# Kernel tuning notes

Measured on AMD Instinct MI355X. Metric: run time of the kernel, lower is better.

## Reference

```python
import jax, jax.numpy as jnp
import numpy as np

H, W, NUM_HEADS = 32, 32, 8


def dwconv3x3(x, w, b):
    # x: (B,C,H,W), w: (C,1,3,3) depthwise, b: (C,)
    y = jax.lax.conv_general_dilated(
        x, w, window_strides=(1, 1), padding='SAME',
        dimension_numbers=('NCHW', 'OIHW', 'NCHW'),
        feature_group_count=x.shape[1])
    return y + b[None, :, None, None]


def conv1x1(x, w, b):
    # x: (B,C,H,W), w: (O,C), b: (O,)
    return jnp.einsum('oc,bchw->bohw', w, x) + b[None, :, None, None]


def layernorm(x, w, b, eps=1e-6):
    mu = x.mean(-1, keepdims=True)
    var = ((x - mu) ** 2).mean(-1, keepdims=True)
    return (x - mu) / jnp.sqrt(var + eps) * w + b


def setup_inputs() -> dict:
    key = jax.random.key(0)
    ks = jax.random.split(key, 12)
    B, N, C = 32, H * W, 512
    Ch = 4 * C  # inverted MLP hidden
    s_lin = 0.02
    s_dw = np.sqrt(2.0 / 9.0)   # fan_out init for 3x3 depthwise
    s_pw1 = np.sqrt(2.0 / Ch)
    s_pw2 = np.sqrt(2.0 / C)
    return {
        'x': jax.random.normal(ks[0], (B, N, C), jnp.float32),
        'cpe_w': jax.random.normal(ks[1], (C, 1, 3, 3), jnp.float32) * s_dw,
        'cpe_b': jnp.zeros((C,), jnp.float32),
        'ln1_w': jnp.ones((C,), jnp.float32),
        'ln1_b': jnp.zeros((C,), jnp.float32),
        'qkv_w': jax.random.normal(ks[2], (3 * C, C), jnp.float32) * s_lin,
        'crpe_w': jax.random.normal(ks[3], (C, 1, 3, 3), jnp.float32) * s_dw,
        'crpe_b': jnp.zeros((C,), jnp.float32),
        'ln2_w': jnp.ones((C,), jnp.float32),
        'ln2_b': jnp.zeros((C,), jnp.float32),
        'fc1_w': jax.random.normal(ks[4], (Ch, C), jnp.float32) * s_pw1,
        'fc1_b': jnp.zeros((Ch,), jnp.float32),
        'dw_w': jax.random.normal(ks[5], (Ch, 1, 3, 3), jnp.float32) * s_dw,
        'dw_b': jnp.zeros((Ch,), jnp.float32),
        'fc2_w': jax.random.normal(ks[6], (C, Ch), jnp.float32) * s_pw2,
        'fc2_b': jnp.zeros((C,), jnp.float32),
    }


def reference(x, cpe_w, cpe_b, ln1_w, ln1_b, qkv_w, crpe_w, crpe_b,
              ln2_w, ln2_b, fc1_w, fc1_b, dw_w, dw_b, fc2_w, fc2_b):
    B, N, C = x.shape
    h = NUM_HEADS
    d = C // h
    scale = d ** -0.5

    # --- Convolutional position encoding: x = x + dwconv(x) ---
    img = x.reshape(B, H, W, C).transpose(0, 3, 1, 2)  # B C H W
    img = img + dwconv3x3(img, cpe_w, cpe_b)
    x = img.transpose(0, 2, 3, 1).reshape(B, N, C)

    # --- Factorized attention + conv relative position encoding ---
    cur = layernorm(x, ln1_w, ln1_b)
    qkv = cur @ qkv_w.T                                 # (B,N,3C)
    qkv = qkv.reshape(B, N, 3, h, d).transpose(2, 0, 3, 1, 4)  # (3,B,h,N,d)
    q, k, v = qkv[0], qkv[1], qkv[2]
    k_softmax = jax.nn.softmax(k, axis=2)               # softmax over tokens N
    ktv = jnp.einsum('bhnk,bhnv->bhkv', k_softmax, v)   # (B,h,d,d)
    factor_att = jnp.einsum('bhnk,bhkv->bhnv', q, ktv)  # (B,h,N,d)
    # crpe: depthwise conv on v as image, elementwise-multiplied by q
    v_img = v.transpose(0, 1, 3, 2).reshape(B, h * d, H, W)
    v_img = dwconv3x3(v_img, crpe_w, crpe_b)
    v_conv = v_img.reshape(B, h, d, N).transpose(0, 1, 3, 2)
    crpe = q * v_conv
    attn_out = (scale * factor_att + crpe).transpose(0, 2, 1, 3).reshape(B, N, C)
    x = x + attn_out

    # --- Inverted MLP (conv-based channel mixing) ---
    cur = layernorm(x, ln2_w, ln2_b)
    img = cur.reshape(B, H, W, C).transpose(0, 3, 1, 2)  # B C H W
    hdn = conv1x1(img, fc1_w, fc1_b)
    hdn = jax.nn.gelu(hdn, approximate=False)
    hdn = hdn + dwconv3x3(hdn, dw_w, dw_b)
    out = conv1x1(hdn, fc2_w, fc2_b)
    x = x + out.transpose(0, 2, 3, 1).reshape(B, N, C)
    return x
```

## Files before the change

### kernel.cpp

```cpp
#include <hip/hip_runtime.h>
#include <hip/hip_bf16.h>

using bf16 = __hip_bfloat16;
using s16x4 = __attribute__((ext_vector_type(4))) short;
using s16x8 = __attribute__((ext_vector_type(8))) short;
using f32x4 = __attribute__((ext_vector_type(4))) float;

#define DI __device__ __forceinline__

template <int N> DI void wvm() {
    if constexpr (N == 8) asm volatile("s_waitcnt vmcnt(8)" ::: "memory");
    else if constexpr (N == 4) asm volatile("s_waitcnt vmcnt(4)" ::: "memory");
    else if constexpr (N == 2) asm volatile("s_waitcnt vmcnt(2)" ::: "memory");
    else if constexpr (N == 1) asm volatile("s_waitcnt vmcnt(1)" ::: "memory");
    else asm volatile("s_waitcnt vmcnt(0)" ::: "memory");
}

DI float b2f(short s) { union { unsigned u; float f; } z; z.u = ((unsigned)(unsigned short)s) << 16; return z.f; }
DI short f2b(float f) { bf16 t = __float2bfloat16(f); return *(short*)&t; }

DI float gelu_f(float x) {
    const float t = 0.7978845608f * x * (1.f + 0.044715f * x * x);
    const float e = __expf(2.f * t);
    const float th = 1.f - 2.f / (e + 1.f);
    return 0.5f * x * (1.f + th);
}

DI void ld8(const bf16* p, float* f) {
    s16x8 x = *(const s16x8*)(const void*)p;
#pragma unroll
    for (int c = 0; c < 8; c++) f[c] = b2f(x[c]);
}
DI void ld8(const float* p, float* f) {
    float4 a = *(const float4*)p, b = *(const float4*)(p + 4);
    f[0]=a.x; f[1]=a.y; f[2]=a.z; f[3]=a.w; f[4]=b.x; f[5]=b.y; f[6]=b.z; f[7]=b.w;
}

typedef const __attribute__((address_space(1))) void* gp_t;
typedef __attribute__((address_space(3))) void* lp_t;
DI void gload_lds16(const void* g, void* l) {
    __builtin_amdgcn_global_load_lds((gp_t)g, (lp_t)l, 16, 0, 0);
}

__global__ void diag_k(float* out, float v) { out[0] = v; }

__global__ void f2bf_k(const float* __restrict__ in, bf16* __restrict__ out, int n) {
    int i = (blockIdx.x * 256 + threadIdx.x) * 8;
    if (i >= n) return;
    float f[8];
    ld8(in + i, f);
    s16x8 o;
#pragma unroll
    for (int c = 0; c < 8; c++) o[c] = f2b(f[c]);
    *(s16x8*)(void*)(out + i) = o;
}

DI void tap10(const float* r, float w0, float w1, float w2, float* acc) {
#pragma unroll
    for (int i = 0; i < 8; i++)
        acc[i] += w0 * r[i] + w1 * r[i + 1] + w2 * r[i + 2];
}

template <typename TI, typename TO, bool RESID, int CPL>
__global__ __launch_bounds__(256) void conv4_k(
    const TI* in, long rs, long coff,
    const float* __restrict__ w, const float* __restrict__ bias,
    TO* out, long ors, int gshift)
{
    constexpr int CH = 64 * CPL;
    constexpr int ECNT = CH / 8;
    __shared__ float buf[2][CH][33];
    const int t = threadIdx.x;
    const int band = blockIdx.x & 3;
    const int cg = (blockIdx.x >> 2) & ((1 << gshift) - 1);
    const int img = blockIdx.x >> (2 + gshift);
    const int y0 = band * 8;

    const int spx = t >> 3;
    const int sce = (t & 7) * ECNT;
    const TI* gsrc = in + ((long)img << 10) * rs + coff + (long)cg * CH + sce;

    const int c = t & 63;
    const int xb = (t >> 6) * 8;

    float wv9[9][CPL], bw[CPL];
#pragma unroll
    for (int p = 0; p < CPL; p++) {
        const int gch = cg * CH + c * CPL + p;
#pragma unroll
        for (int j = 0; j < 9; j++) wv9[j][p] = w[gch * 9 + j];
        bw[p] = bias[gch];
    }

    auto stage = [&](int row) {
        float f[ECNT];
        ld8(gsrc + (long)(row * 32 + spx) * rs, f);
        if constexpr (ECNT == 16) ld8(gsrc + (long)(row * 32 + spx) * rs + 8, f + 8);
        float* d = &buf[row & 1][0][0];
#pragma unroll
        for (int k = 0; k < ECNT; k++) {
            const int ch = sce + k;
            const int rr = (CPL == 2) ? ((ch & 1) * 64 + (ch >> 1)) : ch;
            d[rr * 33 + spx] = f[k];
        }
    };
    auto slice = [&](int row, float r[CPL][10]) {
#pragma unroll
        for (int p = 0; p < CPL; p++) {
            const float* s = &buf[row & 1][c + p * 64][0];
            r[p][0] = (xb == 0) ? 0.f : s[xb - 1];
#pragma unroll
            for (int i = 0; i < 8; i++) r[p][1 + i] = s[xb + i];
            r[p][9] = (xb + 8 >= 32) ? 0.f : s[xb + 8];
        }
    };
    auto zero = [&](float r[CPL][10]) {
#pragma unroll
        for (int p = 0; p < CPL; p++)
#pragma unroll
            for (int i = 0; i < 10; i++) r[p][i] = 0.f;
    };

    float r0[CPL][10], r1[CPL][10], r2[CPL][10];
    if (y0 > 0) stage(y0 - 1);
    __syncthreads();
    if (y0 > 0) slice(y0 - 1, r0); else zero(r0);
    stage(y0);
    __syncthreads();
    slice(y0, r1);

    for (int y = y0; y < y0 + 8; ++y) {
        const int yn = y + 1;
        if (yn <= 31) stage(yn);
        __syncthreads();
        if (yn <= 31) slice(yn, r2); else zero(r2);
        float acc[CPL][8];
#pragma unroll
        for (int p = 0; p < CPL; p++) {
#pragma unroll
            for (int i = 0; i < 8; i++) acc[p][i] = bw[p];
            tap10(r0[p], wv9[0][p], wv9[1][p], wv9[2][p], acc[p]);
            tap10(r1[p], wv9[3][p], wv9[4][p], wv9[5][p], acc[p]);
            tap10(r2[p], wv9[6][p], wv9[7][p], wv9[8][p], acc[p]);
            if (RESID) {
#pragma unroll
                for (int i = 0; i < 8; i++) acc[p][i] += r1[p][i + 1];
            }
        }
        TO* o = out + ((long)(img * 1024 + y * 32 + xb)) * ors + (long)cg * CH + c * CPL;
#pragma unroll
        for (int i = 0; i < 8; i++) {
            if constexpr (CPL == 2 && sizeof(TO) == 2) {
                const unsigned u = (unsigned)(unsigned short)f2b(acc[0][i]) |
                                   ((unsigned)(unsigned short)f2b(acc[1][i]) << 16);
                *(unsigned*)(void*)(o + (long)i * ors) = u;
            } else {
                o[(long)i * ors] = (TO)acc[0][i];
            }
        }
#pragma unroll
        for (int p = 0; p < CPL; p++)
#pragma unroll
            for (int i = 0; i < 10; i++) { r0[p][i] = r1[p][i]; r1[p][i] = r2[p][i]; }
    }
}

__global__ __launch_bounds__(256) void ln_k(const float* __restrict__ x,
                                            const float* __restrict__ w,
                                            const float* __restrict__ bp,
                                            bf16* __restrict__ out)
{
    const size_t row = blockIdx.x * 4 + (threadIdx.x >> 6);
    const int t = threadIdx.x & 63;
    const float* xr = x + row * 512;
    alignas(16) float v[8];
    *(float4*)&v[0] = *(const float4*)(xr + t * 8);
    *(float4*)&v[4] = *(const float4*)(xr + t * 8 + 4);
    float s = 0.f;
#pragma unroll
    for (int j = 0; j < 8; j++) s += v[j];
#pragma unroll
    for (int mm = 32; mm; mm >>= 1) s += __shfl_xor(s, mm);
    const float mu = s * (1.f / 512.f);
    float q = 0.f;
#pragma unroll
    for (int j = 0; j < 8; j++) { v[j] -= mu; q += v[j] * v[j]; }
#pragma unroll
    for (int mm = 32; mm; mm >>= 1) q += __shfl_xor(q, mm);
    const float rstd = rsqrtf(q * (1.f / 512.f) + 1e-6f);
    alignas(16) float wv[8], bv[8];
    *(float4*)&wv[0] = *(const float4*)(w + t * 8);
    *(float4*)&wv[4] = *(const float4*)(w + t * 8 + 4);
    *(float4*)&bv[0] = *(const float4*)(bp + t * 8);
    *(float4*)&bv[4] = *(const float4*)(bp + t * 8 + 4);
    alignas(16) bf16 o[8];
#pragma unroll
    for (int j = 0; j < 8; j++) o[j] = __float2bfloat16(v[j] * rstd * wv[j] + bv[j]);
    *(uint4*)(out + row * 512 + t * 8) = *(const uint4*)o;
}

template <int EPI, int K, int NY>
__global__ __launch_bounds__(512) void gemm8p_k(
    const bf16* __restrict__ A, const bf16* __restrict__ Bw,
    const float* __restrict__ bias, bf16* __restrict__ outb, int M, int Nn)
{
    constexpr int KT = K / 64;
    __shared__ __align__(16) char lds[131072];
    char* ldsA = lds;
    char* ldsB = lds + 65536;
    const int t = threadIdx.x;
    const int lane = t & 63;
    const int w = t >> 6;
    const int wr = w >> 2, wc = w & 3;
    const int nwg = 128 * NY;
    const int swz = (blockIdx.x & 7) * (nwg >> 3) + (blockIdx.x >> 3);
    const int m0 = (swz / NY) * 256;
    const int n0 = (swz % NY) * 256;
    const int lr = lane & 15, lg = lane >> 4;

    f32x4 acc[8][4] = {};

    const int srow = lane >> 3;
    const int ssrc = 8 * ((lane & 7) ^ srow);

    auto SA = [&](int b, int kt, int h) {
#pragma unroll
        for (int j = 0; j < 2; j++) {
            const int lrow0 = j * 64 + w * 8;
            const int R0 = j * 128 + h * 64 + (lrow0 & 63);
            gload_lds16(A + (size_t)(m0 + R0 + srow) * K + kt * 64 + ssrc,
                        ldsA + ((b * 2 + h) * 128 + lrow0) * 128);
        }
    };
    auto SB = [&](int b, int kt, int h) {
#pragma unroll
        for (int j = 0; j < 2; j++) {
            const int lrow0 = j * 64 + w * 8;
            const int R0 = (lrow0 >> 5) * 64 + h * 32 + (lrow0 & 31);
            gload_lds16(Bw + (size_t)(n0 + R0 + srow) * K + kt * 64 + ssrc,
                        ldsB + ((b * 2 + h) * 128 + lrow0) * 128);
        }
    };
    auto RA = [&](int b, int h, int m, int ks) -> s16x8 {
        return *(const s16x8*)(ldsA + ((b * 2 + h) * 128 + wr * 64 + m * 16 + lr) * 128
                               + (((ks * 4 + lg) ^ (lr & 7)) << 4));
    };
    auto RB = [&](int b, int h, int n, int ks) -> s16x8 {
        return *(const s16x8*)(ldsB + ((b * 2 + h) * 128 + wc * 32 + n * 16 + lr) * 128
                               + (((ks * 4 + lg) ^ (lr & 7)) << 4));
    };
    auto MM = [&](int mb, int nb, s16x8 (&a)[2][4], s16x8 (&b)[2][2]) {
#pragma unroll
        for (int ks = 0; ks < 2; ks++)
#pragma unroll
            for (int m = 0; m < 4; m++)
#pragma unroll
                for (int n = 0; n < 2; n++)
                    acc[mb + m][nb + n] =
                        __builtin_amdgcn_mfma_f32_16x16x32_bf16(a[ks][m], b[ks][n], acc[mb + m][nb + n], 0, 0, 0);
    };

    SA(0, 0, 0); SB(0, 0, 0); SA(0, 0, 1); SB(0, 0, 1);
    SA(1, 1, 0); SB(1, 1, 0);
    wvm<8>();
    __builtin_amdgcn_s_barrier();

    s16x8 aLo[2][4], aHi[2][4], bLo[2][2], bHi[2][2];
    auto TILE = [&](int kt) {
        const int b = kt & 1;
#pragma unroll
        for (int ks = 0; ks < 2; ks++) {
#pragma unroll
            for (int m = 0; m < 4; m++) aLo[ks][m] = RA(b, 0, m, ks);
#pragma unroll
            for (int n = 0; n < 2; n++) bLo[ks][n] = RB(b, 0, n, ks);
        }
        if (kt + 1 < KT) SA(b ^ 1, kt + 1, 1);
        __builtin_amdgcn_s_barrier();
        __builtin_amdgcn_s_setprio(1);
        MM(0, 0, aLo, bLo);
        __builtin_amdgcn_s_setprio(0);
        if (kt + 1 < KT) wvm<8>(); else wvm<2>();
        __builtin_amdgcn_s_barrier();
#pragma unroll
        for (int ks = 0; ks < 2; ks++)
#pragma unroll
            for (int m = 0; m < 4; m++) aHi[ks][m] = RA(b, 1, m, ks);
        if (kt + 1 < KT) SB(b ^ 1, kt + 1, 1);
        __builtin_amdgcn_s_barrier();
        __builtin_amdgcn_s_setprio(1);
        MM(4, 0, aHi, bLo);
        __builtin_amdgcn_s_setprio(0);
        if (kt + 1 < KT) wvm<8>(); else wvm<0>();
        __builtin_amdgcn_s_barrier();
#pragma unroll
        for (int ks = 0; ks < 2; ks++)
#pragma unroll
            for (int n = 0; n < 2; n++) bHi[ks][n] = RB(b, 1, n, ks);
        if (kt + 2 < KT) SA(b, kt + 2, 0);
        __builtin_amdgcn_s_barrier();
        __builtin_amdgcn_s_setprio(1);
        MM(4, 2, aHi, bHi);
        __builtin_amdgcn_s_setprio(0);
        __builtin_amdgcn_s_barrier();
        if (kt + 2 < KT) SB(b, kt + 2, 0);
        __builtin_amdgcn_s_barrier();
        __builtin_amdgcn_s_setprio(1);
        MM(0, 2, aLo, bHi);
        __builtin_amdgcn_s_setprio(0);
        if (kt + 2 < KT) { wvm<8>(); __builtin_amdgcn_s_barrier(); }
        else if (kt + 1 < KT) { wvm<4>(); __builtin_amdgcn_s_barrier(); }
    };

#pragma unroll
    for (int kt = 0; kt < KT; ++kt) TILE(kt);

#pragma unroll
    for (int i = 0; i < 8; i++) {
#pragma unroll
        for (int j = 0; j < 4; j++) {
            const int col = n0 + wc * 64 + j * 16 + lr;
            float bcol = 0.f;
            if constexpr (EPI >= 1) bcol = bias[col];
#pragma unroll
            for (int r = 0; r < 4; r++) {
                const int row = m0 + wr * 128 + i * 16 + lg * 4 + r;
                float v = acc[i][j][r] + bcol;
                const size_t idx = (size_t)row * Nn + col;
                outb[idx] = __float2bfloat16(EPI == 1 ? gelu_f(v) : v);
            }
        }
    }
}

__global__ __launch_bounds__(512) void gemm8ps_k(
    const bf16* __restrict__ A, const bf16* __restrict__ A2,
    const bf16* __restrict__ Bw, const float* __restrict__ bias,
    const float* resid, float* outf, int M, int Nn)
{
    constexpr int KT = 32;
    __shared__ __align__(16) char lds[65536];
    char* ldsA = lds;
    char* ldsB = lds + 32768;
    const int t = threadIdx.x;
    const int lane = t & 63;
    const int w = t >> 6;
    const int wr = w >> 2, wc = w & 3;
    const int swz = (blockIdx.x & 7) * 128 + (blockIdx.x >> 3);
    const int m0 = (swz >> 2) * 128;
    const int n0 = (swz & 3) * 128;
    const int lr = lane & 15, lg = lane >> 4;

    f32x4 acc[4][2] = {};

    const int srow = lane >> 3;
    const int ssrc = 8 * ((lane & 7) ^ srow);
    const int lrow0 = w * 8;

    auto SA = [&](int b, int kt, int h) {
        const bf16* Ab = (kt < 16) ? A : A2;
        const int ktl = (kt < 16) ? kt : kt - 16;
        const int R0 = h * 64 + lrow0;
        gload_lds16(Ab + (size_t)(m0 + R0 + srow) * 1024 + ktl * 64 + ssrc,
                    ldsA + ((b * 2 + h) * 64 + lrow0) * 128);
    };
    auto SB = [&](int b, int kt, int h) {
        const int R0 = (lrow0 >> 4) * 32 + h * 16 + (lrow0 & 15);
        gload_lds16(Bw + (size_t)(n0 + R0 + srow) * 2048 + kt * 64 + ssrc,
                    ldsB + ((b * 2 + h) * 64 + lrow0) * 128);
    };
    auto RA = [&](int b, int h, int m, int ks) -> s16x8 {
        return *(const s16x8*)(ldsA + ((b * 2 + h) * 64 + wr * 32 + m * 16 + lr) * 128
                               + (((ks * 4 + lg) ^ (lr & 7)) << 4));
    };
    auto RB = [&](int b, int h, int ks) -> s16x8 {
        return *(const s16x8*)(ldsB + ((b * 2 + h) * 64 + wc * 16 + lr) * 128
                               + (((ks * 4 + lg) ^ (lr & 7)) << 4));
    };
    auto MM = [&](int hm, int hn, s16x8 (&a)[2][2], s16x8 (&bb)[2]) {
#pragma unroll
        for (int ks = 0; ks < 2; ks++)
#pragma unroll
            for (int m = 0; m < 2; m++)
                acc[hm * 2 + m][hn] =
                    __builtin_amdgcn_mfma_f32_16x16x32_bf16(a[ks][m], bb[ks], acc[hm * 2 + m][hn], 0, 0, 0);
    };

    SA(0, 0, 0); SB(0, 0, 0); SA(0, 0, 1); SB(0, 0, 1);
    SA(1, 1, 0); SB(1, 1, 0);
    wvm<4>();
    __builtin_amdgcn_s_barrier();

    s16x8 aLo[2][2], aHi[2][2], bLo[2], bHi[2];
#pragma unroll 2
    for (int kt = 0; kt < KT; ++kt) {
        const int b = kt & 1;
#pragma unroll
        for (int ks = 0; ks < 2; ks++) {
#pragma unroll
            for (int m = 0; m < 2; m++) aLo[ks][m] = RA(b, 0, m, ks);
            bLo[ks] = RB(b, 0, ks);
        }
        if (kt + 1 < KT) SA(b ^ 1, kt + 1, 1);
        __builtin_amdgcn_s_barrier();
        __builtin_amdgcn_s_setprio(1);
        MM(0, 0, aLo, bLo);
        __builtin_amdgcn_s_setprio(0);
        if (kt + 1 < KT) wvm<4>(); else wvm<1>();
        __builtin_amdgcn_s_barrier();
#pragma unroll
        for (int ks = 0; ks < 2; ks++)
#pragma unroll
            for (int m = 0; m < 2; m++) aHi[ks][m] = RA(b, 1, m, ks);
        if (kt + 1 < KT) SB(b ^ 1, kt + 1, 1);
        __builtin_amdgcn_s_barrier();
        __builtin_amdgcn_s_setprio(1);
        MM(1, 0, aHi, bLo);
        __builtin_amdgcn_s_setprio(0);
        if (kt + 1 < KT) wvm<4>(); else wvm<0>();
        __builtin_amdgcn_s_barrier();
#pragma unroll
        for (int ks = 0; ks < 2; ks++) bHi[ks] = RB(b, 1, ks);
        if (kt + 2 < KT) SA(b, kt + 2, 0);
        __builtin_amdgcn_s_barrier();
        __builtin_amdgcn_s_setprio(1);
        MM(1, 1, aHi, bHi);
        __builtin_amdgcn_s_setprio(0);
        __builtin_amdgcn_s_barrier();
        if (kt + 2 < KT) SB(b, kt + 2, 0);
        __builtin_amdgcn_s_barrier();
        __builtin_amdgcn_s_setprio(1);
        MM(0, 1, aLo, bHi);
        __builtin_amdgcn_s_setprio(0);
        if (kt + 2 < KT) { wvm<4>(); __builtin_amdgcn_s_barrier(); }
        else if (kt + 1 < KT) { wvm<2>(); __builtin_amdgcn_s_barrier(); }
    }

#pragma unroll
    for (int mf = 0; mf < 4; mf++) {
#pragma unroll
        for (int nf = 0; nf < 2; nf++) {
            const int col = n0 + wc * 32 + nf * 16 + lr;
            const float bcol = bias[col];
#pragma unroll
            for (int r = 0; r < 4; r++) {
                const int row = m0 + (mf >> 1) * 64 + wr * 32 + (mf & 1) * 16 + lg * 4 + r;
                const size_t idx = (size_t)row * Nn + col;
                outf[idx] = acc[mf][nf][r] + bcol + resid[idx];
            }
        }
    }
}

__global__ __launch_bounds__(256) void ktv3_k(const bf16* __restrict__ qkv,
                                              float* __restrict__ ktvp,
                                              float* __restrict__ csp)
{
    __shared__ __align__(16) char P[64 * 128];
    __shared__ __align__(16) char Vt[64 * 128];
    __shared__ float csl[64 * 5];
    const int t = threadIdx.x;
    const int bh = blockIdx.x >> 1, half = blockIdx.x & 1;
    const int b = bh >> 3, hh = bh & 7;
    const int lane = t & 63, w = t >> 6;
    const int lr = lane & 15, lg = lane >> 4;

    const int n_r = t >> 2;
    const int k0 = (t & 3) * 16;
    const bf16* kbase = qkv + (size_t)(b * 1024) * 1536 + 512 + hh * 64 + k0;
    const bf16* vbase = kbase + 512;

    const int kq = t & 63, qq = t >> 6;
    float cacc = 0.f;

    f32x4 acc[4] = {};

    for (int n0 = half * 512; n0 < half * 512 + 512; n0 += 64) {
        const uint4 ka = *(const uint4*)(kbase + (size_t)(n0 + n_r) * 1536);
        const uint4 kb2 = *(const uint4*)(kbase + (size_t)(n0 + n_r) * 1536 + 8);
        const uint4 va = *(const uint4*)(vbase + (size_t)(n0 + n_r) * 1536);
        const uint4 vb2 = *(const uint4*)(vbase + (size_t)(n0 + n_r) * 1536 + 8);
        __syncthreads();
        {
            const short* ke = (const short*)&ka;
            const short* ke2 = (const short*)&kb2;
            const short* ve = (const short*)&va;
            const short* ve2 = (const short*)&vb2;
            const int nslot = ((n_r >> 3) << 4);
            const int nbyte = (n_r & 7) * 2;
#pragma unroll
            for (int j = 0; j < 16; j++) {
                const int row = k0 + j;
                const short kv = j < 8 ? ke[j] : ke2[j - 8];
                const short vv = j < 8 ? ve[j] : ve2[j - 8];
                const int off = row * 128 + (nslot ^ ((row & 7) << 4)) + nbyte;
                *(short*)(P + off) = f2b(__expf(b2f(kv)));
                *(short*)(Vt + off) = vv;
            }
        }
        __syncthreads();
        {
            const char* pr = P + kq * 128;
            const int sw = (kq & 7) << 4;
            s16x8 x0 = *(const s16x8*)(pr + (((qq * 2) << 4) ^ sw));
            s16x8 x1 = *(const s16x8*)(pr + (((qq * 2 + 1) << 4) ^ sw));
#pragma unroll
            for (int j = 0; j < 8; j++) cacc += b2f(x0[j]) + b2f(x1[j]);
        }
#pragma unroll
        for (int ks2 = 0; ks2 < 2; ks2++) {
            s16x8 aF = *(const s16x8*)(Vt + (w * 16 + lr) * 128 + (((ks2 * 4 + lg) ^ (lr & 7)) << 4));
            s16x8 bF[4];
#pragma unroll
            for (int j = 0; j < 4; j++)
                bF[j] = *(const s16x8*)(P + (j * 16 + lr) * 128 + (((ks2 * 4 + lg) ^ (lr & 7)) << 4));
#pragma unroll
            for (int j = 0; j < 4; j++)
                acc[j] = __builtin_amdgcn_mfma_f32_16x16x32_bf16(aF, bF[j], acc[j], 0, 0, 0);
        }
    }
    __syncthreads();
    csl[kq * 5 + qq] = cacc;
    __syncthreads();
    if (t < 64) csp[blockIdx.x * 64 + t] = csl[t * 5] + csl[t * 5 + 1] + csl[t * 5 + 2] + csl[t * 5 + 3];

    float* o = ktvp + (size_t)blockIdx.x * 4096;
#pragma unroll
    for (int j = 0; j < 4; j++) {
        const int col = j * 16 + lr;
#pragma unroll
        for (int r = 0; r < 4; r++) {
            const int vrow = w * 16 + lg * 4 + r;
            o[vrow * 64 + col] = acc[j][r];
        }
    }
}

__global__ __launch_bounds__(256) void ktvred2_k(const float* __restrict__ ktvp,
                                                 const float* __restrict__ csp,
                                                 bf16* __restrict__ ktvT)
{
    const int bh = blockIdx.x;
    const int t = threadIdx.x;
#pragma unroll
    for (int i = 0; i < 16; i++) {
        const int e = t + 256 * i;
        const int col = e & 63;
        const float cs = csp[(bh * 2) * 64 + col] + csp[(bh * 2 + 1) * 64 + col];
        const float val = ktvp[(size_t)(bh * 2) * 4096 + e] + ktvp[(size_t)(bh * 2 + 1) * 4096 + e];
        ktvT[(size_t)bh * 4096 + e] = __float2bfloat16(val * (0.125f / cs));
    }
}

__global__ __launch_bounds__(256) void attnout2_k(
    float* xs, const bf16* __restrict__ qkv,
    const bf16* __restrict__ ktvT, const bf16* __restrict__ vc)
{
    __shared__ __align__(16) char qs[256 * 128];
    __shared__ __align__(16) char ks[64 * 128];
    const int t = threadIdx.x;
    const int bid = blockIdx.x;
    const int b = bid >> 5, hh = (bid >> 2) & 7, nc = bid & 3;
    const int n0 = nc * 256;
    const int lane = t & 63, w = t >> 6;
    const int lr = lane & 15, lg = lane >> 4;

    {
        const int r0 = t >> 3, sl = t & 7;
#pragma unroll
        for (int it = 0; it < 8; it++) {
            const int row = it * 32 + r0;
            const uint4 v = *(const uint4*)(qkv + ((size_t)(b * 1024 + n0 + row)) * 1536 + hh * 64 + sl * 8);
            *(uint4*)(qs + row * 128 + ((sl ^ (row & 7)) << 4)) = v;
        }
#pragma unroll
        for (int it = 0; it < 2; it++) {
            const int u = it * 256 + t;
            const int vr = u >> 3, sl2 = u & 7;
            const uint4 vv = *(const uint4*)(ktvT + (size_t)(b * 8 + hh) * 4096 + vr * 64 + sl2 * 8);
            *(uint4*)(ks + vr * 128 + ((sl2 ^ (vr & 7)) << 4)) = vv;
        }
    }
    __syncthreads();

    f32x4 acc[4][4] = {};
    s16x8 aF[2][4], bF[2][4];
#pragma unroll
    for (int ksi = 0; ksi < 2; ksi++) {
#pragma unroll
        for (int m = 0; m < 4; m++) {
            const int row = w * 64 + m * 16 + lr;
            aF[ksi][m] = *(const s16x8*)(qs + row * 128 + (((ksi * 4 + lg) ^ (lr & 7)) << 4));
        }
#pragma unroll
        for (int j = 0; j < 4; j++) {
            const int vr = j * 16 + lr;
            bF[ksi][j] = *(const s16x8*)(ks + vr * 128 + (((ksi * 4 + lg) ^ (lr & 7)) << 4));
        }
    }
#pragma unroll
    for (int ksi = 0; ksi < 2; ksi++)
#pragma unroll
        for (int m = 0; m < 4; m++)
#pragma unroll
            for (int j = 0; j < 4; j++)
                acc[m][j] = __builtin_amdgcn_mfma_f32_16x16x32_bf16(aF[ksi][m], bF[ksi][j], acc[m][j], 0, 0, 0);

#pragma unroll
    for (int m = 0; m < 4; m++) {
#pragma unroll
        for (int j = 0; j < 4; j++) {
#pragma unroll
            for (int r = 0; r < 4; r++) {
                const int lrow = w * 64 + m * 16 + lg * 4 + r;
                const int col = j * 16 + lr;
                const size_t idx = ((size_t)(b * 1024 + n0 + lrow)) * 512 + hh * 64 + col;
                const short qv = *(const short*)(qs + lrow * 128 + ((((col >> 3) ^ (lrow & 7)) << 4)) + (col & 7) * 2);
                xs[idx] = xs[idx] + acc[m][j][r] + b2f(qv) * __bfloat162float(vc[idx]);
            }
        }
    }
}

static constexpr size_t OFF_WQ   = 0;
static constexpr size_t OFF_W1   = 1572864;
static constexpr size_t OFF_W2   = 3670016;
static constexpr size_t OFF_CUR  = 5767168;
static constexpr size_t OFF_H2B  = 5767168;
static constexpr size_t OFF_QKV  = 72876032;
static constexpr size_t OFF_HG   = 72876032;
static constexpr size_t OFF_VC   = 173539328;
static constexpr size_t OFF_KTVP = 173539328;
static constexpr size_t OFF_CSP  = 181927936;
static constexpr size_t OFF_H2A  = 139984896;
static constexpr size_t OFF_KTV  = 207093760;
static constexpr size_t WS_NEED  = 207618048;

extern "C" void kernel_launch(void* const* d_in, const int* in_sizes, int n_in,
                              void* d_out, int out_size, void* d_ws, size_t ws_size,
                              hipStream_t stream)
{
    const float* x     = (const float*)d_in[0];
    const float* cpe_w = (const float*)d_in[1];
    const float* cpe_b = (const float*)d_in[2];
    const float* ln1_w = (const float*)d_in[3];
    const float* ln1_b = (const float*)d_in[4];
    const float* qkv_w = (const float*)d_in[5];
    const float* crpe_w= (const float*)d_in[6];
    const float* crpe_b= (const float*)d_in[7];
    const float* ln2_w = (const float*)d_in[8];
    const float* ln2_b = (const float*)d_in[9];
    const float* fc1_w = (const float*)d_in[10];
    const float* fc1_b = (const float*)d_in[11];
    const float* dw_w  = (const float*)d_in[12];
    const float* dw_b  = (const float*)d_in[13];
    const float* fc2_w = (const float*)d_in[14];
    const float* fc2_b = (const float*)d_in[15];
    float* spine = (float*)d_out;
    char* ws = (char*)d_ws;

    if (ws_size < WS_NEED) {
        diag_k<<<1, 1, 0, stream>>>(spine, (float)ws_size);
        return;
    }

    bf16*  wq   = (bf16*)(ws + OFF_WQ);
    bf16*  w1   = (bf16*)(ws + OFF_W1);
    bf16*  w2b  = (bf16*)(ws + OFF_W2);
    bf16*  cur  = (bf16*)(ws + OFF_CUR);
    bf16*  qkv  = (bf16*)(ws + OFF_QKV);
    bf16*  vc   = (bf16*)(ws + OFF_VC);
    float* ktvp = (float*)(ws + OFF_KTVP);
    float* csp  = (float*)(ws + OFF_CSP);
    bf16*  ktvT = (bf16*)(ws + OFF_KTV);
    bf16*  hg   = (bf16*)(ws + OFF_HG);
    bf16*  h2a  = (bf16*)(ws + OFF_H2A);
    bf16*  h2b  = (bf16*)(ws + OFF_H2B);

    f2bf_k<<<(1536 * 512 / 8 + 255) / 256, 256, 0, stream>>>(qkv_w, wq, 1536 * 512);
    f2bf_k<<<(2048 * 512 / 8 + 255) / 256, 256, 0, stream>>>(fc1_w, w1, 2048 * 512);
    f2bf_k<<<(2048 * 512 / 8 + 255) / 256, 256, 0, stream>>>(fc2_w, w2b, 512 * 2048);

    conv4_k<float, float, true, 1><<<32 * 8 * 4, 256, 0, stream>>>(x, 512, 0, cpe_w, cpe_b, spine, 512, 3);

    const int M = 32768;
    ln_k<<<M / 4, 256, 0, stream>>>(spine, ln1_w, ln1_b, cur);
    gemm8p_k<0, 512, 6><<<768, 512, 0, stream>>>(cur, wq, nullptr, qkv, M, 1536);
    ktv3_k<<<512, 256, 0, stream>>>(qkv, ktvp, csp);
    ktvred2_k<<<256, 256, 0, stream>>>(ktvp, csp, ktvT);
    conv4_k<bf16, bf16, false, 2><<<32 * 4 * 4, 256, 0, stream>>>(qkv, 1536, 1024, crpe_w, crpe_b, vc, 512, 2);
    attnout2_k<<<32 * 8 * 4, 256, 0, stream>>>(spine, qkv, ktvT, vc);
    ln_k<<<M / 4, 256, 0, stream>>>(spine, ln2_w, ln2_b, cur);

    gemm8p_k<1, 512, 4><<<512, 512, 0, stream>>>(cur, w1, fc1_b, hg, M, 1024);
    conv4_k<bf16, bf16, true, 2><<<32 * 8 * 4, 256, 0, stream>>>(hg, 1024, 0, dw_w, dw_b, h2a, 1024, 3);
    gemm8p_k<1, 512, 4><<<512, 512, 0, stream>>>(cur, w1 + (size_t)1024 * 512, fc1_b + 1024, hg, M, 1024);
    conv4_k<bf16, bf16, true, 2><<<32 * 8 * 4, 256, 0, stream>>>(hg, 1024, 0, dw_w + (size_t)1024 * 9, dw_b + 1024, h2b, 1024, 3);
    gemm8ps_k<<<1024, 512, 0, stream>>>(h2a, h2b, w2b, fc2_b, spine, spine, M, 512);
}
```

Before: 466.6 us.

## Generalize split-K GEMM for fc1 tiles and fold KtV reduction into attention output

Templates the 128x128 gemm8ps kernel over epilogue, K, tile grid and dual-A input, and uses it for both fc1 GEMMs with 2048 workgroups in place of the larger-tile kernel. Removes the separate ktvred kernel: attnout now sums the two partial KtV halves and normalizes by the column sums while loading into LDS. This drops a launch and a bf16 intermediate, but repeats the reduction work in every block that touches the same head. Workspace offsets for the partials now alias the cur buffer, which relies on kernel ordering.

Measured after the change: 465.6 us. About the same (-0.2%).

```diff
diff --git a/kernel.cpp b/kernel.cpp
--- a/kernel.cpp
+++ b/kernel.cpp
@@ -333,12 +333,14 @@
     }
 }
 
+template <int EPI, int K, int NY, bool DUAL>
 __global__ __launch_bounds__(512) void gemm8ps_k(
     const bf16* __restrict__ A, const bf16* __restrict__ A2,
     const bf16* __restrict__ Bw, const float* __restrict__ bias,
-    const float* resid, float* outf, int M, int Nn)
+    const float* resid, bf16* __restrict__ outb, float* outf, int M, int Nn)
 {
-    constexpr int KT = 32;
+    constexpr int KT = K / 64;
+    constexpr int LDA = DUAL ? K / 2 : K;
     __shared__ __align__(16) char lds[65536];
     char* ldsA = lds;
     char* ldsB = lds + 32768;
@@ -346,9 +348,10 @@
     const int lane = t & 63;
     const int w = t >> 6;
     const int wr = w >> 2, wc = w & 3;
-    const int swz = (blockIdx.x & 7) * 128 + (blockIdx.x >> 3);
-    const int m0 = (swz >> 2) * 128;
-    const int n0 = (swz & 3) * 128;
+    const int nwg = gridDim.x;
+    const int swz = (blockIdx.x & 7) * (nwg >> 3) + (blockIdx.x >> 3);
+    const int m0 = (swz / NY) * 128;
+    const int n0 = (swz % NY) * 128;
     const int lr = lane & 15, lg = lane >> 4;
 
     f32x4 acc[4][2] = {};
@@ -358,15 +361,16 @@
     const int lrow0 = w * 8;
 
     auto SA = [&](int b, int kt, int h) {
-        const bf16* Ab = (kt < 16) ? A : A2;
-        const int ktl = (kt < 16) ? kt : kt - 16;
+        const bf16* Ab = A;
+        int ktl = kt;
+        if constexpr (DUAL) { if (kt >= KT / 2) { Ab = A2; ktl = kt - KT / 2; } }
         const int R0 = h * 64 + lrow0;
-        gload_lds16(Ab + (size_t)(m0 + R0 + srow) * 1024 + ktl * 64 + ssrc,
+        gload_lds16(Ab + (size_t)(m0 + R0 + srow) * LDA + ktl * 64 + ssrc,
                     ldsA + ((b * 2 + h) * 64 + lrow0) * 128);
     };
     auto SB = [&](int b, int kt, int h) {
         const int R0 = (lrow0 >> 4) * 32 + h * 16 + (lrow0 & 15);
-        gload_lds16(Bw + (size_t)(n0 + R0 + srow) * 2048 + kt * 64 + ssrc,
+        gload_lds16(Bw + (size_t)(n0 + R0 + srow) * K + kt * 64 + ssrc,
                     ldsB + ((b * 2 + h) * 64 + lrow0) * 128);
     };
     auto RA = [&](int b, int h, int m, int ks) -> s16x8 {
@@ -441,12 +445,15 @@
 #pragma unroll
         for (int nf = 0; nf < 2; nf++) {
             const int col = n0 + wc * 32 + nf * 16 + lr;
-            const float bcol = bias[col];
+            float bcol = 0.f;
+            if constexpr (EPI >= 1) bcol = bias[col];
 #pragma unroll
             for (int r = 0; r < 4; r++) {
                 const int row = m0 + (mf >> 1) * 64 + wr * 32 + (mf & 1) * 16 + lg * 4 + r;
+                float v = acc[mf][nf][r] + bcol;
                 const size_t idx = (size_t)row * Nn + col;
-                outf[idx] = acc[mf][nf][r] + bcol + resid[idx];
+                if (EPI == 2) outf[idx] = v + resid[idx];
+                else outb[idx] = __float2bfloat16(EPI == 1 ? gelu_f(v) : v);
             }
         }
     }
@@ -536,31 +543,17 @@
     }
 }
 
-__global__ __launch_bounds__(256) void ktvred2_k(const float* __restrict__ ktvp,
-                                                 const float* __restrict__ csp,
-                                                 bf16* __restrict__ ktvT)
-{
-    const int bh = blockIdx.x;
-    const int t = threadIdx.x;
-#pragma unroll
-    for (int i = 0; i < 16; i++) {
-        const int e = t + 256 * i;
-        const int col = e & 63;
-        const float cs = csp[(bh * 2) * 64 + col] + csp[(bh * 2 + 1) * 64 + col];
-        const float val = ktvp[(size_t)(bh * 2) * 4096 + e] + ktvp[(size_t)(bh * 2 + 1) * 4096 + e];
-        ktvT[(size_t)bh * 4096 + e] = __float2bfloat16(val * (0.125f / cs));
-    }
-}
-
-__global__ __launch_bounds__(256) void attnout2_k(
+__global__ __launch_bounds__(256) void attnout3_k(
     float* xs, const bf16* __restrict__ qkv,
-    const bf16* __restrict__ ktvT, const bf16* __restrict__ vc)
+    const float* __restrict__ ktvp, const float* __restrict__ csp,
+    const bf16* __restrict__ vc)
 {
     __shared__ __align__(16) char qs[256 * 128];
     __shared__ __align__(16) char ks[64 * 128];
     const int t = threadIdx.x;
     const int bid = blockIdx.x;
     const int b = bid >> 5, hh = (bid >> 2) & 7, nc = bid & 3;
+    const int bh = b * 8 + hh;
     const int n0 = nc * 256;
     const int lane = t & 63, w = t >> 6;
     const int lr = lane & 15, lg = lane >> 4;
@@ -577,8 +570,16 @@
         for (int it = 0; it < 2; it++) {
             const int u = it * 256 + t;
             const int vr = u >> 3, sl2 = u & 7;
-            const uint4 vv = *(const uint4*)(ktvT + (size_t)(b * 8 + hh) * 4096 + vr * 64 + sl2 * 8);
-            *(uint4*)(ks + vr * 128 + ((sl2 ^ (vr & 7)) << 4)) = vv;
+            const float* p0 = ktvp + (size_t)(bh * 2) * 4096 + vr * 64 + sl2 * 8;
+            const float* p1 = p0 + 4096;
+            s16x8 o;
+#pragma unroll
+            for (int j = 0; j < 8; j++) {
+                const int col = sl2 * 8 + j;
+                const float cs = csp[(bh * 2) * 64 + col] + csp[(bh * 2 + 1) * 64 + col];
+                o[j] = f2b((p0[j] + p1[j]) * (0.125f / cs));
+            }
+            *(s16x8*)(void*)(ks + vr * 128 + ((sl2 ^ (vr & 7)) << 4)) = o;
         }
     }
     __syncthreads();
@@ -627,13 +628,12 @@
 static constexpr size_t OFF_W2   = 3670016;
 static constexpr size_t OFF_CUR  = 5767168;
 static constexpr size_t OFF_H2B  = 5767168;
+static constexpr size_t OFF_KTVP = 5767168;
+static constexpr size_t OFF_CSP  = 14155776;
 static constexpr size_t OFF_QKV  = 72876032;
 static constexpr size_t OFF_HG   = 72876032;
 static constexpr size_t OFF_VC   = 173539328;
-static constexpr size_t OFF_KTVP = 173539328;
-static constexpr size_t OFF_CSP  = 181927936;
 static constexpr size_t OFF_H2A  = 139984896;
-static constexpr size_t OFF_KTV  = 207093760;
 static constexpr size_t WS_NEED  = 207618048;
 
 extern "C" void kernel_launch(void* const* d_in, const int* in_sizes, int n_in,
@@ -672,7 +672,6 @@
     bf16*  vc   = (bf16*)(ws + OFF_VC);
     float* ktvp = (float*)(ws + OFF_KTVP);
     float* csp  = (float*)(ws + OFF_CSP);
-    bf16*  ktvT = (bf16*)(ws + OFF_KTV);
     bf16*  hg   = (bf16*)(ws + OFF_HG);
     bf16*  h2a  = (bf16*)(ws + OFF_H2A);
     bf16*  h2b  = (bf16*)(ws + OFF_H2B);
@@ -687,14 +686,13 @@
     ln_k<<<M / 4, 256, 0, stream>>>(spine, ln1_w, ln1_b, cur);
     gemm8p_k<0, 512, 6><<<768, 512, 0, stream>>>(cur, wq, nullptr, qkv, M, 1536);
     ktv3_k<<<512, 256, 0, stream>>>(qkv, ktvp, csp);
-    ktvred2_k<<<256, 256, 0, stream>>>(ktvp, csp, ktvT);
     conv4_k<bf16, bf16, false, 2><<<32 * 4 * 4, 256, 0, stream>>>(qkv, 1536, 1024, crpe_w, crpe_b, vc, 512, 2);
-    attnout2_k<<<32 * 8 * 4, 256, 0, stream>>>(spine, qkv, ktvT, vc);
+    attnout3_k<<<32 * 8 * 4, 256, 0, stream>>>(spine, qkv, ktvp, csp, vc);
     ln_k<<<M / 4, 256, 0, stream>>>(spine, ln2_w, ln2_b, cur);
 
-    gemm8p_k<1, 512, 4><<<512, 512, 0, stream>>>(cur, w1, fc1_b, hg, M, 1024);
+    gemm8ps_k<1, 512, 8, false><<<2048, 512, 0, stream>>>(cur, nullptr, w1, fc1_b, nullptr, hg, nullptr, M, 1024);
     conv4_k<bf16, bf16, true, 2><<<32 * 8 * 4, 256, 0, stream>>>(hg, 1024, 0, dw_w, dw_b, h2a, 1024, 3);
-    gemm8p_k<1, 512, 4><<<512, 512, 0, stream>>>(cur, w1 + (size_t)1024 * 512, fc1_b + 1024, hg, M, 1024);
+    gemm8ps_k<1, 512, 8, false><<<2048, 512, 0, stream>>>(cur, nullptr, w1 + (size_t)1024 * 512, fc1_b + 1024, nullptr, hg, nullptr, M, 1024);
     conv4_k<bf16, bf16, true, 2><<<32 * 8 * 4, 256, 0, stream>>>(hg, 1024, 0, dw_w + (size_t)1024 * 9, dw_b + 1024, h2b, 1024, 3);
-    gemm8ps_k<<<1024, 512, 0, stream>>>(h2a, h2b, w2b, fc2_b, spine, spine, M, 512);
-}
+    gemm8ps_k<2, 2048, 4, true><<<1024, 512, 0, stream>>>(h2a, h2b, w2b, fc2_b, spine, nullptr, spine, M, 512);
+}
```
